# Performance work log

Measured on AMD Instinct MI355X. Metric: run time of the kernel, lower is better.

## Reference

```python
import jax, jax.numpy as jnp
import numpy as np

C = 128; PE = 8; WALK = 20; NODE_F = 28; EDGE_F = 4
L = 4; H = 4; DH = C // H; B = 64; NPG = 512; N = B * NPG; E = 262144
BN_EPS = 1e-5


def _bn(x, g, b):
    # BatchNorm1d, training-mode statistics (biased var), over the node axis
    m = x.mean(0)
    v = x.var(0)
    return (x - m) * jax.lax.rsqrt(v + BN_EPS) * g + b


def _forward(pe, node_emb, pe_lin_w, pe_lin_b, pe_norm_g, pe_norm_b, edge_emb,
             gine_w1, gine_b1, gine_w2, gine_b2,
             attn_wqkv, attn_bqkv, attn_wo, attn_bo,
             norm1_g, norm1_b, norm2_g, norm2_b, norm3_g, norm3_b,
             ffn_w1, ffn_b1, ffn_w2, ffn_b2,
             mlp_w1, mlp_b1, mlp_w2, mlp_b2, mlp_w3, mlp_b3,
             x, edge_index, edge_attr, batch):
    pe_n = _bn(pe, pe_norm_g, pe_norm_b)
    h = jnp.concatenate([node_emb[x[:, 0]], pe_n @ pe_lin_w + pe_lin_b], axis=1)  # [N, C]
    ea = edge_emb[edge_attr]  # [E, C]
    src, dst = edge_index[0], edge_index[1]
    scale = 1.0 / jnp.sqrt(jnp.asarray(DH, h.dtype))
    for l in range(L):
        # --- GINEConv: nn((1+eps)*x + sum_{j->i} relu(x_j + e_ji)), eps=0 ---
        msg = jax.nn.relu(h[src] + ea)                      # [E, C] gather
        agg = jax.ops.segment_sum(msg, dst, num_segments=N) # [N, C] scatter-add
        z = agg + h
        local = jax.nn.relu(z @ gine_w1[l] + gine_b1[l]) @ gine_w2[l] + gine_b2[l]
        h_loc = _bn(local + h, norm1_g[l], norm1_b[l])
        # --- global multihead attention on dense batch [B, NPG, C] (equal-size graphs) ---
        xd = h.reshape(B, NPG, C)
        qkv = xd @ attn_wqkv[l] + attn_bqkv[l]              # [B, NPG, 3C]
        q, k, v = jnp.split(qkv, 3, axis=-1)
        q = q.reshape(B, NPG, H, DH)
        k = k.reshape(B, NPG, H, DH)
        v = v.reshape(B, NPG, H, DH)
        att = jax.nn.softmax(jnp.einsum('bqhd,bkhd->bhqk', q, k) * scale, axis=-1)
        o = jnp.einsum('bhqk,bkhd->bqhd', att, v).reshape(B, NPG, C) @ attn_wo[l] + attn_bo[l]
        h_att = _bn(o.reshape(N, C) + h, norm2_g[l], norm2_b[l])
        # --- combine + FFN (GPSConv) ---
        out = h_loc + h_att
        ffn = jax.nn.relu(out @ ffn_w1[l] + ffn_b1[l]) @ ffn_w2[l] + ffn_b2[l]
        h = _bn(out + ffn, norm3_g[l], norm3_b[l])
    g = jax.ops.segment_sum(h, batch, num_segments=B)       # global_add_pool -> [B, C]
    y = jax.nn.relu(g @ mlp_w1 + mlp_b1)
    y = jax.nn.relu(y @ mlp_w2 + mlp_b2)
    return y @ mlp_w3 + mlp_b3                              # [B, 1]


def setup_inputs() -> dict:
    key = jax.random.key(0)
    ks = iter(jax.random.split(key, 48))
    def w(shape, s=0.05):
        return jax.random.normal(next(ks), shape, jnp.float32) * s
    inp = {}
    inp['x'] = jax.random.randint(next(ks), (N, 1), 0, NODE_F)
    inp['pe'] = jax.random.normal(next(ks), (N, WALK), jnp.float32)
    inp['edge_index'] = jax.random.randint(next(ks), (2, E), 0, N)
    inp['edge_attr'] = jax.random.randint(next(ks), (E,), 0, EDGE_F)
    inp['batch'] = jnp.arange(N, dtype=jnp.int32) // NPG
    inp['node_emb'] = w((NODE_F, C - PE), 1.0)
    inp['pe_lin_w'] = w((WALK, PE))
    inp['pe_lin_b'] = jnp.zeros((PE,), jnp.float32)
    inp['pe_norm_g'] = jnp.ones((WALK,), jnp.float32)
    inp['pe_norm_b'] = jnp.zeros((WALK,), jnp.float32)
    inp['edge_emb'] = w((EDGE_F, C), 1.0)
    inp['gine_w1'] = w((L, C, C))
    inp['gine_b1'] = jnp.zeros((L, C), jnp.float32)
    inp['gine_w2'] = w((L, C, C))
    inp['gine_b2'] = jnp.zeros((L, C), jnp.float32)
    inp['attn_wqkv'] = w((L, C, 3 * C))
    inp['attn_bqkv'] = jnp.zeros((L, 3 * C), jnp.float32)
    inp['attn_wo'] = w((L, C, C))
    inp['attn_bo'] = jnp.zeros((L, C), jnp.float32)
    for nm in ('norm1', 'norm2', 'norm3'):
        inp[nm + '_g'] = jnp.ones((L, C), jnp.float32)
        inp[nm + '_b'] = jnp.zeros((L, C), jnp.float32)
    inp['ffn_w1'] = w((L, C, 2 * C))
    inp['ffn_b1'] = jnp.zeros((L, 2 * C), jnp.float32)
    inp['ffn_w2'] = w((L, 2 * C, C))
    inp['ffn_b2'] = jnp.zeros((L, C), jnp.float32)
    inp['mlp_w1'] = w((C, C // 2))
    inp['mlp_b1'] = jnp.zeros((C // 2,), jnp.float32)
    inp['mlp_w2'] = w((C // 2, C // 4))
    inp['mlp_b2'] = jnp.zeros((C // 4,), jnp.float32)
    inp['mlp_w3'] = w((C // 4, 1))
    inp['mlp_b3'] = jnp.zeros((1,), jnp.float32)
    return inp


def reference(x, pe, edge_index, edge_attr, batch,
              node_emb, pe_lin_w, pe_lin_b, pe_norm_g, pe_norm_b, edge_emb,
              gine_w1, gine_b1, gine_w2, gine_b2,
              attn_wqkv, attn_bqkv, attn_wo, attn_bo,
              norm1_g, norm1_b, norm2_g, norm2_b, norm3_g, norm3_b,
              ffn_w1, ffn_b1, ffn_w2, ffn_b2,
              mlp_w1, mlp_b1, mlp_w2, mlp_b2, mlp_w3, mlp_b3):
    return _forward(pe, node_emb, pe_lin_w, pe_lin_b, pe_norm_g, pe_norm_b, edge_emb,
                    gine_w1, gine_b1, gine_w2, gine_b2,
                    attn_wqkv, attn_bqkv, attn_wo, attn_bo,
                    norm1_g, norm1_b, norm2_g, norm2_b, norm3_g, norm3_b,
                    ffn_w1, ffn_b1, ffn_w2, ffn_b2,
                    mlp_w1, mlp_b1, mlp_w2, mlp_b2, mlp_w3, mlp_b3,
                    x, edge_index, edge_attr, batch)
```

## Files before the change

kernel.cpp:

```cpp
#include <hip/hip_runtime.h>
#include <math.h>
#include <cstddef>

#define N_NODES 32768
#define C_DIM   128
#define E_EDGES 262144
#define B_GR    64
#define NPG     512
#define WALK_D  20
#define L_LAYERS 4

static constexpr int NF = N_NODES * C_DIM;

typedef __attribute__((ext_vector_type(8))) short bf16x8;
typedef __attribute__((ext_vector_type(4))) float f32x4;
typedef __attribute__((ext_vector_type(4))) short short4v;

__device__ inline unsigned short f2bf(float f)
{
    union { float f; unsigned u; } v; v.f = f;
    unsigned r = v.u + 0x7fff + ((v.u >> 16) & 1);
    return (unsigned short)(r >> 16);
}
__device__ inline float bf2f_lo(unsigned u) { return __uint_as_float(u << 16); }
__device__ inline float bf2f_hi(unsigned u) { return __uint_as_float(u & 0xffff0000u); }
__device__ inline unsigned cvt_pk_bf16(float lo, float hi)
{
    unsigned r;
    asm("v_cvt_pk_bf16_f32 %0, %1, %2" : "=v"(r) : "v"(lo), "v"(hi));
    return r;
}

__global__ __launch_bounds__(256) void pe_stats_k(const float* __restrict__ pe, float* __restrict__ acc)
{
    int gt = blockIdx.x * 256 + threadIdx.x;
    float s[WALK_D], q[WALK_D];
    #pragma unroll
    for (int c = 0; c < WALK_D; ++c) { s[c] = 0.f; q[c] = 0.f; }
    for (int r = 0; r < 4; ++r) {
        const float* row = &pe[(size_t)(gt + r * 8192) * WALK_D];
        float v[20];
        #pragma unroll
        for (int j = 0; j < 5; ++j) *(float4*)&v[j * 4] = *(const float4*)(row + j * 4);
        #pragma unroll
        for (int c = 0; c < WALK_D; ++c) { s[c] += v[c]; q[c] += v[c] * v[c]; }
    }
    #pragma unroll
    for (int c = 0; c < WALK_D; ++c) {
        float ss = s[c], qq = q[c];
        #pragma unroll
        for (int m = 1; m < 64; m <<= 1) { ss += __shfl_xor(ss, m); qq += __shfl_xor(qq, m); }
        if ((threadIdx.x & 63) == 0) { atomicAdd(&acc[c], ss); atomicAdd(&acc[32 + c], qq); }
    }
}

__global__ __launch_bounds__(256) void h0_k(const int* __restrict__ x, const float* __restrict__ pe,
    const float* __restrict__ node_emb, const float* __restrict__ plw, const float* __restrict__ plb,
    const float* __restrict__ peacc, const float* __restrict__ pe_g, const float* __restrict__ pe_b,
    float* __restrict__ h, unsigned short* __restrict__ h16)
{
    __shared__ float spe[64];
    int tid = threadIdx.x;
    if (tid < WALK_D) {
        float mean = peacc[tid] * (1.f / N_NODES);
        float var  = peacc[32 + tid] * (1.f / N_NODES) - mean * mean;
        float sc   = pe_g[tid] * rsqrtf(var + 1e-5f);
        spe[tid] = sc;
        spe[32 + tid] = pe_b[tid] - mean * sc;
    }
    __syncthreads();
    int i = blockIdx.x * 2 + (tid >> 7);
    int c = tid & 127;
    float v;
    if (c < 120) {
        v = node_emb[x[i] * 120 + c];
    } else {
        int pc = c - 120;
        v = plb[pc];
        #pragma unroll
        for (int k = 0; k < WALK_D; ++k) {
            float pn = pe[i * WALK_D + k] * spe[k] + spe[32 + k];
            v = fmaf(pn, plw[k * 8 + pc], v);
        }
    }
    h[i * C_DIM + c] = v;
    h16[i * C_DIM + c] = f2bf(v);
}

__global__ __launch_bounds__(256) void hist_k(const int* __restrict__ dst, int* __restrict__ cnt)
{
    int e = blockIdx.x * 256 + threadIdx.x;
    atomicAdd(&cnt[dst[e]], 1);
}

__global__ __launch_bounds__(256) void bsum_k(const int* __restrict__ cnt, int* __restrict__ bsum)
{
    __shared__ int ws[4];
    int b = blockIdx.x, t = threadIdx.x;
    int v = cnt[b * 256 + t];
    #pragma unroll
    for (int m = 1; m < 64; m <<= 1) v += __shfl_xor(v, m);
    if ((t & 63) == 0) ws[t >> 6] = v;
    __syncthreads();
    if (t == 0) bsum[b] = ws[0] + ws[1] + ws[2] + ws[3];
}

__global__ __launch_bounds__(128) void bscan_k(const int* __restrict__ bsum, int* __restrict__ bpre)
{
    __shared__ int s[128];
    int t = threadIdx.x;
    int v = bsum[t];
    s[t] = v;
    __syncthreads();
    for (int off = 1; off < 128; off <<= 1) {
        int u = (t >= off) ? s[t - off] : 0;
        __syncthreads();
        s[t] += u;
        __syncthreads();
    }
    bpre[t] = s[t] - v;
}

__global__ __launch_bounds__(256) void indptr_k(const int* __restrict__ cnt, const int* __restrict__ bpre,
                                                int* __restrict__ indptr)
{
    __shared__ int s[256];
    int b = blockIdx.x, t = threadIdx.x;
    int v = cnt[b * 256 + t];
    s[t] = v;
    __syncthreads();
    for (int off = 1; off < 256; off <<= 1) {
        int u = (t >= off) ? s[t - off] : 0;
        __syncthreads();
        s[t] += u;
        __syncthreads();
    }
    indptr[b * 256 + t] = bpre[b] + s[t] - v;
    if (b == 127 && t == 255) indptr[N_NODES] = E_EDGES;
}

__global__ __launch_bounds__(256) void scatter_k(const int* __restrict__ dst, const int* __restrict__ src,
                                                 const int* __restrict__ attr, const int* __restrict__ indptr,
                                                 int* __restrict__ cur, int* __restrict__ esa)
{
    int e = blockIdx.x * 256 + threadIdx.x;
    int d = dst[e];
    int pos = atomicAdd(&cur[d], 1);
    esa[indptr[d] + pos] = src[e] | (attr[e] << 16);
}

__global__ __launch_bounds__(256) void gine_gather_k(const unsigned short* __restrict__ h16,
    const int* __restrict__ esa, const int* __restrict__ indptr,
    const float* __restrict__ edge_emb, unsigned short* __restrict__ z16)
{
    __shared__ float ee[4 * C_DIM];
    int tid = threadIdx.x;
    ee[tid] = edge_emb[tid];
    ee[tid + 256] = edge_emb[tid + 256];
    __syncthreads();
    int i = blockIdx.x * 4 + (tid >> 6);
    int c = (tid & 63) * 2;
    int p0 = indptr[i], p1 = indptr[i + 1];
    float s0 = 0.f, s1 = 0.f;
    int p = p0;
    for (; p + 4 <= p1; p += 4) {
        int sa0 = esa[p], sa1 = esa[p + 1], sa2 = esa[p + 2], sa3 = esa[p + 3];
        unsigned u0 = *(const unsigned*)&h16[(size_t)(sa0 & 0xffff) * C_DIM + c];
        unsigned u1 = *(const unsigned*)&h16[(size_t)(sa1 & 0xffff) * C_DIM + c];
        unsigned u2 = *(const unsigned*)&h16[(size_t)(sa2 & 0xffff) * C_DIM + c];
        unsigned u3 = *(const unsigned*)&h16[(size_t)(sa3 & 0xffff) * C_DIM + c];
        float2 e0 = *(const float2*)&ee[(sa0 >> 16) * C_DIM + c];
        float2 e1 = *(const float2*)&ee[(sa1 >> 16) * C_DIM + c];
        float2 e2 = *(const float2*)&ee[(sa2 >> 16) * C_DIM + c];
        float2 e3 = *(const float2*)&ee[(sa3 >> 16) * C_DIM + c];
        s0 += fmaxf(bf2f_lo(u0) + e0.x, 0.f); s1 += fmaxf(bf2f_hi(u0) + e0.y, 0.f);
        s0 += fmaxf(bf2f_lo(u1) + e1.x, 0.f); s1 += fmaxf(bf2f_hi(u1) + e1.y, 0.f);
        s0 += fmaxf(bf2f_lo(u2) + e2.x, 0.f); s1 += fmaxf(bf2f_hi(u2) + e2.y, 0.f);
        s0 += fmaxf(bf2f_lo(u3) + e3.x, 0.f); s1 += fmaxf(bf2f_hi(u3) + e3.y, 0.f);
    }
    for (; p < p1; ++p) {
        int sa = esa[p];
        unsigned u = *(const unsigned*)&h16[(size_t)(sa & 0xffff) * C_DIM + c];
        float2 ev = *(const float2*)&ee[(sa >> 16) * C_DIM + c];
        s0 += fmaxf(bf2f_lo(u) + ev.x, 0.f);
        s1 += fmaxf(bf2f_hi(u) + ev.y, 0.f);
    }
    unsigned us = *(const unsigned*)&h16[(size_t)i * C_DIM + c];
    s0 += bf2f_lo(us);
    s1 += bf2f_hi(us);
    *(unsigned*)&z16[(size_t)i * C_DIM + c] = cvt_pk_bf16(s0, s1);
}

__global__ __launch_bounds__(256) void wt_prep_k(
    const float* __restrict__ gw1, const float* __restrict__ gw2,
    const float* __restrict__ wqkv, const float* __restrict__ wo,
    const float* __restrict__ fw1, const float* __restrict__ fw2,
    short* __restrict__ out)
{
    __shared__ float ts[32][36];
    int b = blockIdx.x;
    int l = b / 160, t = b % 160;
    const float* src; int K, N; size_t obase; int tile;
    if (t < 16)       { src = gw1  + (size_t)l * 16384; K = 128; N = 128; obase = (size_t)l * 163840 + 0;      tile = t; }
    else if (t < 32)  { src = gw2  + (size_t)l * 16384; K = 128; N = 128; obase = (size_t)l * 163840 + 16384;  tile = t - 16; }
    else if (t < 80)  { src = wqkv + (size_t)l * 49152; K = 128; N = 384; obase = (size_t)l * 163840 + 32768;  tile = t - 32; }
    else if (t < 96)  { src = wo   + (size_t)l * 16384; K = 128; N = 128; obase = (size_t)l * 163840 + 81920;  tile = t - 80; }
    else if (t < 128) { src = fw1  + (size_t)l * 32768; K = 128; N = 256; obase = (size_t)l * 163840 + 98304;  tile = t - 96; }
    else              { src = fw2  + (size_t)l * 32768; K = 256; N = 128; obase = (size_t)l * 163840 + 131072; tile = t - 128; }
    int ntN = N / 32;
    int tk = tile / ntN, tn = tile % ntN;
    int tid = threadIdx.x;
    int r = tid >> 3, c4 = (tid & 7) * 4;
    *(float4*)&ts[r][c4] = *(const float4*)&src[(size_t)(tk * 32 + r) * N + tn * 32 + c4];
    __syncthreads();
    int n = tid >> 3, k4 = (tid & 7) * 4;
    short4v pk;
    #pragma unroll
    for (int i2 = 0; i2 < 4; ++i2) pk[i2] = (short)f2bf(ts[k4 + i2][n]);
    *(short4v*)&out[obase + (size_t)(tn * 32 + n) * K + tk * 32 + k4] = pk;
}

template<int KD, int NC, int AMODE, int RESMODE, bool RELU, bool STATS, bool OUTBF, bool ABF, bool VOUT>
__global__ __launch_bounds__(256) void mgemm_k(
    const void* __restrict__ Av, const float* __restrict__ A2,
    const float* __restrict__ affA1, const float* __restrict__ affA2,
    const unsigned short* __restrict__ Bt, const float* __restrict__ bias,
    const float* __restrict__ R1, const float* __restrict__ R2,
    const float* __restrict__ affR1, const float* __restrict__ affR2,
    void* __restrict__ Cout, float* __restrict__ stats,
    unsigned short* __restrict__ vtg)
{
    __shared__ short As[16384];
    __shared__ short Bs[8192];
    const int tid = threadIdx.x;
    const int w = tid >> 6;
    const int lane = tid & 63;
    const int lr = lane & 15, lg = lane >> 4;
    const int row0 = blockIdx.y * 128;
    const int col0 = blockIdx.x * 128;

    const f32x4 zero = {0.f, 0.f, 0.f, 0.f};
    f32x4 acc[2][8];
    #pragma unroll
    for (int i = 0; i < 2; ++i)
        #pragma unroll
        for (int cf = 0; cf < 8; ++cf) acc[i][cf] = zero;

    for (int kt = 0; kt < KD / 128; ++kt) {
        if (kt > 0) __syncthreads();
        #pragma unroll
        for (int it = 0; it < 8; ++it) {
            int gid = it * 256 + tid;
            int row = gid >> 4, g = gid & 15;
            bf16x8 pk;
            if (ABF) {
                pk = *(const bf16x8*)&((const unsigned short*)Av)[(size_t)(row0 + row) * KD + kt * 128 + g * 8];
            } else {
                const float* Af = (const float*)Av;
                const float* ap = &Af[(size_t)(row0 + row) * KD + kt * 128 + g * 8];
                float v[8];
                *(float4*)&v[0] = *(const float4*)ap;
                *(float4*)&v[4] = *(const float4*)(ap + 4);
                if (AMODE == 1) {
                    const float* ap2 = &A2[(size_t)(row0 + row) * KD + kt * 128 + g * 8];
                    float u[8];
                    *(float4*)&u[0] = *(const float4*)ap2;
                    *(float4*)&u[4] = *(const float4*)(ap2 + 4);
                    #pragma unroll
                    for (int j = 0; j < 8; ++j) {
                        int ck = g * 8 + j;
                        v[j] = v[j] * affA1[ck] + affA1[128 + ck] + u[j] * affA2[ck] + affA2[128 + ck];
                    }
                }
                #pragma unroll
                for (int j = 0; j < 8; ++j) pk[j] = (short)f2bf(v[j]);
            }
            *(bf16x8*)&As[(row * 16 + (g ^ (row & 7))) * 8] = pk;
        }
        #pragma unroll
        for (int h = 0; h < 2; ++h) {
            if (h > 0) __syncthreads();
            #pragma unroll
            for (int it = 0; it < 4; ++it) {
                int gid = it * 256 + tid;
                int row = gid >> 4, g = gid & 15;
                bf16x8 bv = *(const bf16x8*)&Bt[(size_t)(col0 + h * 64 + row) * KD + kt * 128 + g * 8];
                *(bf16x8*)&Bs[(row * 16 + (g ^ (row & 7))) * 8] = bv;
            }
            __syncthreads();
            #pragma unroll
            for (int ks = 0; ks < 4; ++ks) {
                bf16x8 af[2], bfr[4];
                #pragma unroll
                for (int i = 0; i < 2; ++i) {
                    int row = w * 32 + i * 16 + lr;
                    int g = ks * 4 + lg;
                    af[i] = *(const bf16x8*)&As[(row * 16 + (g ^ (row & 7))) * 8];
                }
                #pragma unroll
                for (int cfl = 0; cfl < 4; ++cfl) {
                    int lc = cfl * 16 + lr;
                    int g = ks * 4 + lg;
                    bfr[cfl] = *(const bf16x8*)&Bs[(lc * 16 + (g ^ (lc & 7))) * 8];
                }
                #pragma unroll
                for (int i = 0; i < 2; ++i)
                    #pragma unroll
                    for (int cfl = 0; cfl < 4; ++cfl)
                        acc[i][h * 4 + cfl] = __builtin_amdgcn_mfma_f32_16x16x32_bf16(af[i], bfr[cfl], acc[i][h * 4 + cfl], 0, 0, 0);
            }
        }
    }

    float* cs = (float*)As;
    float* cq = cs + 128;
    if (STATS) {
        __syncthreads();
        if (tid < 128) { cs[tid] = 0.f; cq[tid] = 0.f; }
        __syncthreads();
    }
    float bs_v[8];
    #pragma unroll
    for (int cf = 0; cf < 8; ++cf) bs_v[cf] = bias[col0 + cf * 16 + lr];
    float rs1[8], ro1[8], rs2[8], ro2[8];
    if (RESMODE == 2) {
        #pragma unroll
        for (int cf = 0; cf < 8; ++cf) {
            int c = cf * 16 + lr;
            rs1[cf] = affR1[c]; ro1[cf] = affR1[128 + c];
            rs2[cf] = affR2[c]; ro2[cf] = affR2[128 + c];
        }
    }
    float colS[8], colQ[8];
    #pragma unroll
    for (int cf = 0; cf < 8; ++cf) { colS[cf] = 0.f; colQ[cf] = 0.f; }
    const bool vblk = VOUT && (col0 == 256);
    #pragma unroll
    for (int i = 0; i < 2; ++i) {
        #pragma unroll
        for (int r = 0; r < 4; ++r) {
            size_t grow = row0 + w * 32 + i * 16 + lg * 4 + r;
            #pragma unroll
            for (int cf = 0; cf < 8; ++cf) {
                int c = col0 + cf * 16 + lr;
                float val = acc[i][cf][r] + bs_v[cf];
                if (RESMODE == 1) val += R1[grow * NC + c];
                if (RESMODE == 2) {
                    val += R1[grow * 128 + c] * rs1[cf] + ro1[cf]
                         + R2[grow * 128 + c] * rs2[cf] + ro2[cf];
                }
                if (RELU) val = fmaxf(val, 0.f);
                if (VOUT && vblk) {
                    int g2 = (int)(grow >> 9);
                    int key = (int)(grow & 511);
                    int kc = key >> 6, kg = (key >> 3) & 7, j = key & 7;
                    int cd = c - 256;
                    int hd2 = cd >> 5, dd = cd & 31;
                    vtg[((size_t)(g2 * 4 + hd2) * 8 + kc) * 2048 + dd * 64 + ((kg ^ (dd & 7)) << 3) + j] = f2bf(val);
                } else if (OUTBF) {
                    ((unsigned short*)Cout)[grow * NC + c] = f2bf(val);
                } else {
                    ((float*)Cout)[grow * NC + c] = val;
                }
                if (STATS) { colS[cf] += val; colQ[cf] += val * val; }
            }
        }
    }
    if (STATS) {
        #pragma unroll
        for (int cf = 0; cf < 8; ++cf) {
            float s = colS[cf], q = colQ[cf];
            s += __shfl_xor(s, 16); s += __shfl_xor(s, 32);
            q += __shfl_xor(q, 16); q += __shfl_xor(q, 32);
            if (lg == 0) { atomicAdd(&cs[cf * 16 + lr], s); atomicAdd(&cq[cf * 16 + lr], q); }
        }
        __syncthreads();
        if (tid < 128) {
            atomicAdd(&stats[tid], cs[tid]);
            atomicAdd(&stats[128 + tid], cq[tid]);
        }
    }
}

__global__ __launch_bounds__(512) void gine_mlp_k(
    const unsigned short* __restrict__ z16,
    const unsigned short* __restrict__ W1t, const float* __restrict__ b1,
    const unsigned short* __restrict__ W2t, const float* __restrict__ b2,
    const float* __restrict__ Hres,
    float* __restrict__ T1out, float* __restrict__ stats)
{
    __shared__ short As[16384];
    __shared__ short Bs[16384];
    const int tid = threadIdx.x;
    const int w = tid >> 6;
    const int lane = tid & 63;
    const int lr = lane & 15, lg = lane >> 4;
    const int row0 = blockIdx.x * 128;
    const f32x4 zero = {0.f, 0.f, 0.f, 0.f};
    const int arow = w * 16 + lr;

    #pragma unroll
    for (int it = 0; it < 4; ++it) {
        int gid = it * 512 + tid;
        int row = gid >> 4, g = gid & 15;
        bf16x8 av = *(const bf16x8*)&z16[(size_t)(row0 + row) * 128 + g * 8];
        *(bf16x8*)&As[(row * 16 + (g ^ (row & 7))) * 8] = av;
        bf16x8 bv = *(const bf16x8*)&W1t[(size_t)row * 128 + g * 8];
        *(bf16x8*)&Bs[(row * 16 + (g ^ (row & 7))) * 8] = bv;
    }
    __syncthreads();

    f32x4 acc[8];
    #pragma unroll
    for (int cf = 0; cf < 8; ++cf) acc[cf] = zero;
    #pragma unroll
    for (int ks = 0; ks < 4; ++ks) {
        int g = ks * 4 + lg;
        bf16x8 af = *(const bf16x8*)&As[(arow * 16 + (g ^ (arow & 7))) * 8];
        #pragma unroll
        for (int cf = 0; cf < 8; ++cf) {
            int c = cf * 16 + lr;
            bf16x8 bfr = *(const bf16x8*)&Bs[(c * 16 + (g ^ (c & 7))) * 8];
            acc[cf] = __builtin_amdgcn_mfma_f32_16x16x32_bf16(af, bfr, acc[cf], 0, 0, 0);
        }
    }
    __syncthreads();

    {
        float bias1[8];
        #pragma unroll
        for (int cf = 0; cf < 8; ++cf) bias1[cf] = b1[cf * 16 + lr];
        #pragma unroll
        for (int r = 0; r < 4; ++r) {
            int row = w * 16 + lg * 4 + r;
            #pragma unroll
            for (int cf = 0; cf < 8; ++cf) {
                int col = cf * 16 + lr;
                float val = fmaxf(acc[cf][r] + bias1[cf], 0.f);
                As[(row * 16 + ((col >> 3) ^ (row & 7))) * 8 + (col & 7)] = (short)f2bf(val);
            }
        }
    }
    #pragma unroll
    for (int it = 0; it < 4; ++it) {
        int gid = it * 512 + tid;
        int row = gid >> 4, g = gid & 15;
        bf16x8 bv = *(const bf16x8*)&W2t[(size_t)row * 128 + g * 8];
        *(bf16x8*)&Bs[(row * 16 + (g ^ (row & 7))) * 8] = bv;
    }
    __syncthreads();

    #pragma unroll
    for (int cf = 0; cf < 8; ++cf) acc[cf] = zero;
    #pragma unroll
    for (int ks = 0; ks < 4; ++ks) {
        int g = ks * 4 + lg;
        bf16x8 af = *(const bf16x8*)&As[(arow * 16 + (g ^ (arow & 7))) * 8];
        #pragma unroll
        for (int cf = 0; cf < 8; ++cf) {
            int c = cf * 16 + lr;
            bf16x8 bfr = *(const bf16x8*)&Bs[(c * 16 + (g ^ (c & 7))) * 8];
            acc[cf] = __builtin_amdgcn_mfma_f32_16x16x32_bf16(af, bfr, acc[cf], 0, 0, 0);
        }
    }

    float* cs = (float*)As;
    float* cq = cs + 128;
    __syncthreads();
    if (tid < 128) { cs[tid] = 0.f; cq[tid] = 0.f; }
    __syncthreads();
    float bs_v[8];
    #pragma unroll
    for (int cf = 0; cf < 8; ++cf) bs_v[cf] = b2[cf * 16 + lr];
    float colS[8], colQ[8];
    #pragma unroll
    for (int cf = 0; cf < 8; ++cf) { colS[cf] = 0.f; colQ[cf] = 0.f; }
    #pragma unroll
    for (int r = 0; r < 4; ++r) {
        size_t grow = row0 + w * 16 + lg * 4 + r;
        #pragma unroll
        for (int cf = 0; cf < 8; ++cf) {
            int c = cf * 16 + lr;
            float val = acc[cf][r] + bs_v[cf] + Hres[grow * 128 + c];
            T1out[grow * 128 + c] = val;
            colS[cf] += val; colQ[cf] += val * val;
        }
    }
    #pragma unroll
    for (int cf = 0; cf < 8; ++cf) {
        float s = colS[cf], q = colQ[cf];
        s += __shfl_xor(s, 16); s += __shfl_xor(s, 32);
        q += __shfl_xor(q, 16); q += __shfl_xor(q, 32);
        if (lg == 0) { atomicAdd(&cs[cf * 16 + lr], s); atomicAdd(&cq[cf * 16 + lr], q); }
    }
    __syncthreads();
    if (tid < 128) {
        atomicAdd(&stats[tid], cs[tid]);
        atomicAdd(&stats[128 + tid], cq[tid]);
    }
}

__global__ __launch_bounds__(256) void ffn_mlp_k(
    const float* __restrict__ T1, const float* __restrict__ T2,
    const float* __restrict__ a1, const float* __restrict__ g1v, const float* __restrict__ b1v,
    const float* __restrict__ a2, const float* __restrict__ g2v, const float* __restrict__ b2v,
    const unsigned short* __restrict__ W1t, const float* __restrict__ fb1,
    const unsigned short* __restrict__ W2t, const float* __restrict__ fb2,
    float* __restrict__ T1out, float* __restrict__ stats)
{
    __shared__ short As[8192];
    __shared__ short Bs[16384];
    __shared__ short Ys[8192];
    __shared__ float sf1l[256], sf2l[256];
    const int tid = threadIdx.x;
    const int w = tid >> 6;
    const int lane = tid & 63;
    const int lr = lane & 15, lg = lane >> 4;
    const int row0 = blockIdx.x * 64;
    const f32x4 zero = {0.f, 0.f, 0.f, 0.f};

    if (tid < 128) {
        float mean = a1[tid] * (1.f / N_NODES);
        float var  = a1[128 + tid] * (1.f / N_NODES) - mean * mean;
        float sc   = g1v[tid] * rsqrtf(var + 1e-5f);
        sf1l[tid] = sc; sf1l[128 + tid] = b1v[tid] - mean * sc;
        mean = a2[tid] * (1.f / N_NODES);
        var  = a2[128 + tid] * (1.f / N_NODES) - mean * mean;
        sc   = g2v[tid] * rsqrtf(var + 1e-5f);
        sf2l[tid] = sc; sf2l[128 + tid] = b2v[tid] - mean * sc;
    }
    __syncthreads();

    #pragma unroll
    for (int it = 0; it < 4; ++it) {
        int gid = it * 256 + tid;
        int row = gid >> 4, g = gid & 15;
        const float* ap = &T1[(size_t)(row0 + row) * 128 + g * 8];
        const float* ap2 = &T2[(size_t)(row0 + row) * 128 + g * 8];
        float v[8], u[8];
        *(float4*)&v[0] = *(const float4*)ap;
        *(float4*)&v[4] = *(const float4*)(ap + 4);
        *(float4*)&u[0] = *(const float4*)ap2;
        *(float4*)&u[4] = *(const float4*)(ap2 + 4);
        unsigned pw[4];
        #pragma unroll
        for (int j2 = 0; j2 < 4; ++j2) {
            int ck0 = g * 8 + j2 * 2, ck1 = ck0 + 1;
            float x0 = v[j2 * 2]     * sf1l[ck0] + sf1l[128 + ck0] + u[j2 * 2]     * sf2l[ck0] + sf2l[128 + ck0];
            float x1 = v[j2 * 2 + 1] * sf1l[ck1] + sf1l[128 + ck1] + u[j2 * 2 + 1] * sf2l[ck1] + sf2l[128 + ck1];
            pw[j2] = cvt_pk_bf16(x0, x1);
        }
        *(uint4*)&As[(row * 16 + (g ^ (row & 7))) * 8] = *(uint4*)pw;
    }

    f32x4 acc2[8];
    #pragma unroll
    for (int cf = 0; cf < 8; ++cf) acc2[cf] = zero;

    const int arow = w * 16 + lr;
    for (int h = 0; h < 2; ++h) {
        if (h > 0) __syncthreads();
        #pragma unroll
        for (int it = 0; it < 8; ++it) {
            int gid = it * 256 + tid;
            int row = gid >> 4, g = gid & 15;
            bf16x8 bv = *(const bf16x8*)&W1t[(size_t)(h * 128 + row) * 128 + g * 8];
            *(bf16x8*)&Bs[(row * 16 + (g ^ (row & 7))) * 8] = bv;
        }
        __syncthreads();
        f32x4 accY[8];
        #pragma unroll
        for (int cf = 0; cf < 8; ++cf) accY[cf] = zero;
        #pragma unroll
        for (int ks = 0; ks < 4; ++ks) {
            int g = ks * 4 + lg;
            bf16x8 af = *(const bf16x8*)&As[(arow * 16 + (g ^ (arow & 7))) * 8];
            #pragma unroll
            for (int cf = 0; cf < 8; ++cf) {
                int c = cf * 16 + lr;
                bf16x8 bfr = *(const bf16x8*)&Bs[(c * 16 + (g ^ (c & 7))) * 8];
                accY[cf] = __builtin_amdgcn_mfma_f32_16x16x32_bf16(af, bfr, accY[cf], 0, 0, 0);
            }
        }
        __syncthreads();
        #pragma unroll
        for (int r = 0; r < 4; ++r) {
            int row = w * 16 + lg * 4 + r;
            #pragma unroll
            for (int cf = 0; cf < 8; ++cf) {
                int col = cf * 16 + lr;
                float val = fmaxf(accY[cf][r] + fb1[h * 128 + col], 0.f);
                Ys[(row * 16 + ((col >> 3) ^ (row & 7))) * 8 + (col & 7)] = (short)f2bf(val);
            }
        }
        #pragma unroll
        for (int it = 0; it < 8; ++it) {
            int gid = it * 256 + tid;
            int row = gid >> 4, g = gid & 15;
            bf16x8 bv = *(const bf16x8*)&W2t[(size_t)row * 256 + h * 128 + g * 8];
            *(bf16x8*)&Bs[(row * 16 + (g ^ (row & 7))) * 8] = bv;
        }
        __syncthreads();
        #pragma unroll
        for (int ks = 0; ks < 4; ++ks) {
            int g = ks * 4 + lg;
            bf16x8 af = *(const bf16x8*)&Ys[(arow * 16 + (g ^ (arow & 7))) * 8];
            #pragma unroll
            for (int cf = 0; cf < 8; ++cf) {
                int c = cf * 16 + lr;
                bf16x8 bfr = *(const bf16x8*)&Bs[(c * 16 + (g ^ (c & 7))) * 8];
                acc2[cf] = __builtin_amdgcn_mfma_f32_16x16x32_bf16(af, bfr, acc2[cf], 0, 0, 0);
            }
        }
    }

    float* cs = (float*)As;
    float* cq = cs + 128;
    __syncthreads();
    if (tid < 128) { cs[tid] = 0.f; cq[tid] = 0.f; }
    __syncthreads();
    float bs_v[8], rs1[8], ro1[8], rs2[8], ro2[8];
    #pragma unroll
    for (int cf = 0; cf < 8; ++cf) {
        int c = cf * 16 + lr;
        bs_v[cf] = fb2[c];
        rs1[cf] = sf1l[c]; ro1[cf] = sf1l[128 + c];
        rs2[cf] = sf2l[c]; ro2[cf] = sf2l[128 + c];
    }
    float colS[8], colQ[8];
    #pragma unroll
    for (int cf = 0; cf < 8; ++cf) { colS[cf] = 0.f; colQ[cf] = 0.f; }
    #pragma unroll
    for (int r = 0; r < 4; ++r) {
        size_t grow = row0 + w * 16 + lg * 4 + r;
        #pragma unroll
        for (int cf = 0; cf < 8; ++cf) {
            int c = cf * 16 + lr;
            float val = acc2[cf][r] + bs_v[cf]
                      + T1[grow * 128 + c] * rs1[cf] + ro1[cf]
                      + T2[grow * 128 + c] * rs2[cf] + ro2[cf];
            T1out[grow * 128 + c] = val;
            colS[cf] += val; colQ[cf] += val * val;
        }
    }
    #pragma unroll
    for (int cf = 0; cf < 8; ++cf) {
        float s = colS[cf], q = colQ[cf];
        s += __shfl_xor(s, 16); s += __shfl_xor(s, 32);
        q += __shfl_xor(q, 16); q += __shfl_xor(q, 32);
        if (lg == 0) { atomicAdd(&cs[cf * 16 + lr], s); atomicAdd(&cq[cf * 16 + lr], q); }
    }
    __syncthreads();
    if (tid < 128) {
        atomicAdd(&stats[tid], cs[tid]);
        atomicAdd(&stats[128 + tid], cq[tid]);
    }
}

__global__ __launch_bounds__(256) void attn_mfma_k(const unsigned short* __restrict__ qkvb,
                                                   const unsigned short* __restrict__ vtg,
                                                   unsigned short* __restrict__ ao16)
{
    __shared__ short Qs[2048];
    __shared__ short Ks[2][2048];
    __shared__ short Vs[2][2048];
    __shared__ short Ps[4][1024];
    const int tid = threadIdx.x;
    const int w = tid >> 6, lane = tid & 63;
    const int lr = lane & 15, lg = lane >> 4;
    const int q0 = blockIdx.x * 64;
    const int hd = blockIdx.y;
    const int base = blockIdx.z * NPG;
    const float SCL = 0.17677669529663687f * 1.44269504089f;
    const f32x4 zero = {0.f, 0.f, 0.f, 0.f};
    const unsigned short* vbase = vtg + (size_t)(blockIdx.z * 4 + hd) * 16384;

    {
        int row = tid >> 2, g = tid & 3;
        bf16x8 qv = *(const bf16x8*)&qkvb[(size_t)(base + q0 + row) * 384 + hd * 32 + g * 8];
        *(bf16x8*)&Qs[(row * 4 + (g ^ ((row >> 1) & 3))) * 8] = qv;
        bf16x8 kv = *(const bf16x8*)&qkvb[(size_t)(base + row) * 384 + 128 + hd * 32 + g * 8];
        *(bf16x8*)&Ks[0][(row * 4 + (g ^ ((row >> 1) & 3))) * 8] = kv;
        bf16x8 vv = *(const bf16x8*)&vbase[tid * 8];
        *(bf16x8*)&Vs[0][tid * 8] = vv;
    }
    __syncthreads();
    const int qrow = w * 16 + lr;
    const bf16x8 bq = *(const bf16x8*)&Qs[(qrow * 4 + (lg ^ ((qrow >> 1) & 3))) * 8];
    float m = -1e30f, lsum = 0.f;
    f32x4 o[2];
    o[0] = zero; o[1] = zero;

    for (int kc = 0; kc < 8; ++kc) {
        int buf = kc & 1;
        bf16x8 knx, vnx;
        if (kc < 7) {
            int row = tid >> 2, g = tid & 3;
            knx = *(const bf16x8*)&qkvb[(size_t)(base + (kc + 1) * 64 + row) * 384 + 128 + hd * 32 + g * 8];
            vnx = *(const bf16x8*)&vbase[(size_t)(kc + 1) * 2048 + tid * 8];
        }
        bf16x8 ka[4], va[2][2];
        #pragma unroll
        for (int kf = 0; kf < 4; ++kf) {
            int kr = kf * 16 + lr;
            ka[kf] = *(const bf16x8*)&Ks[buf][(kr * 4 + (lg ^ ((kr >> 1) & 3))) * 8];
        }
        #pragma unroll
        for (int ks = 0; ks < 2; ++ks)
            #pragma unroll
            for (int df = 0; df < 2; ++df) {
                int d = df * 16 + lr;
                int kg = ks * 4 + lg;
                va[ks][df] = *(const bf16x8*)&Vs[buf][(d * 8 + (kg ^ (d & 7))) * 8];
            }
        f32x4 s[4];
        #pragma unroll
        for (int kf = 0; kf < 4; ++kf)
            s[kf] = __builtin_amdgcn_mfma_f32_16x16x32_bf16(ka[kf], bq, zero, 0, 0, 0);
        float v[16];
        #pragma unroll
        for (int kf = 0; kf < 4; ++kf)
            #pragma unroll
            for (int r = 0; r < 4; ++r) v[kf * 4 + r] = s[kf][r] * SCL;
        float rm = fmaxf(fmaxf(fmaxf(fmaxf(v[0], v[1]), fmaxf(v[2], v[3])),
                               fmaxf(fmaxf(v[4], v[5]), fmaxf(v[6], v[7]))),
                         fmaxf(fmaxf(fmaxf(v[8], v[9]), fmaxf(v[10], v[11])),
                               fmaxf(fmaxf(v[12], v[13]), fmaxf(v[14], v[15]))));
        rm = fmaxf(rm, __shfl_xor(rm, 16));
        rm = fmaxf(rm, __shfl_xor(rm, 32));
        float mn = fmaxf(m, rm);
        float alpha = exp2f(m - mn);
        float p[16];
        #pragma unroll
        for (int i = 0; i < 16; ++i) p[i] = exp2f(v[i] - mn);
        float S0 = ((p[0] + p[4]) + p[8]) + p[12];
        float S1 = ((p[1] + p[5]) + p[9]) + p[13];
        float S2 = ((p[2] + p[6]) + p[10]) + p[14];
        float S3 = ((p[3] + p[7]) + p[11]) + p[15];
        float ps = (S0 + S1) + (S2 + S3);
        ps += __shfl_xor(ps, 16);
        ps += __shfl_xor(ps, 32);
        lsum = lsum * alpha + ps;
        m = mn;
        o[0] *= alpha;
        o[1] *= alpha;
        #pragma unroll
        for (int kf = 0; kf < 4; ++kf) {
            uint2 pk;
            pk.x = cvt_pk_bf16(p[kf * 4 + 0], p[kf * 4 + 1]);
            pk.y = cvt_pk_bf16(p[kf * 4 + 2], p[kf * 4 + 3]);
            int gr = (kf * 2 + (lg >> 1)) ^ (lr & 7);
            *(uint2*)&Ps[w][lr * 64 + gr * 8 + (lg & 1) * 4] = pk;
        }
        #pragma unroll
        for (int ks = 0; ks < 2; ++ks) {
            bf16x8 pa = *(const bf16x8*)&Ps[w][lr * 64 + (((ks * 4 + lg) ^ (lr & 7))) * 8];
            #pragma unroll
            for (int df = 0; df < 2; ++df)
                o[df] = __builtin_amdgcn_mfma_f32_16x16x32_bf16(va[ks][df], pa, o[df], 0, 0, 0);
        }
        if (kc < 7) {
            int row = tid >> 2, g = tid & 3;
            *(bf16x8*)&Ks[buf ^ 1][(row * 4 + (g ^ ((row >> 1) & 3))) * 8] = knx;
            *(bf16x8*)&Vs[buf ^ 1][tid * 8] = vnx;
        }
        __syncthreads();
    }
    {
        float inv = 1.f / lsum;
        size_t nrow = (size_t)base + q0 + w * 16 + lr;
        #pragma unroll
        for (int df = 0; df < 2; ++df) {
            uint2 ov;
            ov.x = cvt_pk_bf16(o[df][0] * inv, o[df][1] * inv);
            ov.y = cvt_pk_bf16(o[df][2] * inv, o[df][3] * inv);
            *(uint2*)&ao16[nrow * 128 + hd * 32 + df * 16 + lg * 4] = ov;
        }
    }
}

__global__ __launch_bounds__(256) void bn_apply_k(const float* __restrict__ t,
    const float* __restrict__ a3, const float* __restrict__ g3, const float* __restrict__ b3,
    float* __restrict__ h, unsigned short* __restrict__ h16)
{
    __shared__ float sfl[256];
    int tid = threadIdx.x;
    if (tid < 128) {
        float mean = a3[tid] * (1.f / N_NODES);
        float var  = a3[128 + tid] * (1.f / N_NODES) - mean * mean;
        float sc   = g3[tid] * rsqrtf(var + 1e-5f);
        sfl[tid] = sc;
        sfl[128 + tid] = b3[tid] - mean * sc;
    }
    __syncthreads();
    int idx = blockIdx.x * 256 + tid;
    int cg = (idx & 31) * 4;
    float4 v  = *(const float4*)&t[idx * 4];
    float4 sc = *(const float4*)&sfl[cg];
    float4 sh = *(const float4*)&sfl[128 + cg];
    float4 o;
    o.x = v.x * sc.x + sh.x;
    o.y = v.y * sc.y + sh.y;
    o.z = v.z * sc.z + sh.z;
    o.w = v.w * sc.w + sh.w;
    *(float4*)&h[idx * 4] = o;
    uint2 p;
    p.x = cvt_pk_bf16(o.x, o.y);
    p.y = cvt_pk_bf16(o.z, o.w);
    *(uint2*)&h16[idx * 4] = p;
}

__global__ __launch_bounds__(128) void pool_k(const float* __restrict__ h, float* __restrict__ g)
{
    int b = blockIdx.x, c = threadIdx.x;
    float s = 0.f;
    for (int i = 0; i < NPG; ++i) s += h[(size_t)((b << 9) + i) * C_DIM + c];
    g[b * C_DIM + c] = s;
}

__global__ __launch_bounds__(256) void head_mlp_k(const float* __restrict__ g,
    const float* __restrict__ w1, const float* __restrict__ b1,
    const float* __restrict__ w2, const float* __restrict__ b2,
    const float* __restrict__ w3, const float* __restrict__ b3,
    float* __restrict__ out)
{
    __shared__ float gs[64 * 128];
    __shared__ float y1[64 * 64];
    __shared__ float y2[64 * 32];
    int tid = threadIdx.x;
    for (int r = 0; r < 32; ++r) gs[r * 256 + tid] = g[r * 256 + tid];
    __syncthreads();
    for (int t = 0; t < 16; ++t) {
        int idx = t * 256 + tid;
        int gi = idx >> 6, c = idx & 63;
        float s = b1[c];
        for (int k = 0; k < 128; ++k) s = fmaf(gs[gi * 128 + k], w1[k * 64 + c], s);
        y1[gi * 64 + c] = fmaxf(s, 0.f);
    }
    __syncthreads();
    for (int t = 0; t < 8; ++t) {
        int idx = t * 256 + tid;
        int gi = idx >> 5, c = idx & 31;
        float s = b2[c];
        for (int k = 0; k < 64; ++k) s = fmaf(y1[gi * 64 + k], w2[k * 32 + c], s);
        y2[gi * 32 + c] = fmaxf(s, 0.f);
    }
    __syncthreads();
    if (tid < 64) {
        float s = b3[0];
        for (int k = 0; k < 32; ++k) s = fmaf(y2[tid * 32 + k], w3[k], s);
        out[tid] = s;
    }
}

extern "C" void kernel_launch(void* const* d_in, const int* in_sizes, int n_in,
                              void* d_out, int out_size, void* d_ws, size_t ws_size,
                              hipStream_t stream)
{
    const int*   x        = (const int*)  d_in[0];
    const float* pe       = (const float*)d_in[1];
    const int*   ei       = (const int*)  d_in[2];
    const int*   eattr    = (const int*)  d_in[3];
    const float* node_emb = (const float*)d_in[5];
    const float* plw      = (const float*)d_in[6];
    const float* plb      = (const float*)d_in[7];
    const float* pe_g     = (const float*)d_in[8];
    const float* pe_b     = (const float*)d_in[9];
    const float* edge_emb = (const float*)d_in[10];
    const float* gw1      = (const float*)d_in[11];
    const float* gb1      = (const float*)d_in[12];
    const float* gw2      = (const float*)d_in[13];
    const float* gb2      = (const float*)d_in[14];
    const float* wqkv     = (const float*)d_in[15];
    const float* bqkv     = (const float*)d_in[16];
    const float* wo       = (const float*)d_in[17];
    const float* bo       = (const float*)d_in[18];
    const float* n1g      = (const float*)d_in[19];
    const float* n1b      = (const float*)d_in[20];
    const float* n2g      = (const float*)d_in[21];
    const float* n2b      = (const float*)d_in[22];
    const float* n3g      = (const float*)d_in[23];
    const float* n3b      = (const float*)d_in[24];
    const float* fw1      = (const float*)d_in[25];
    const float* fb1      = (const float*)d_in[26];
    const float* fw2      = (const float*)d_in[27];
    const float* fb2      = (const float*)d_in[28];
    const float* mw1      = (const float*)d_in[29];
    const float* mb1      = (const float*)d_in[30];
    const float* mw2      = (const float*)d_in[31];
    const float* mb2      = (const float*)d_in[32];
    const float* mw3      = (const float*)d_in[33];
    const float* mb3      = (const float*)d_in[34];

    float* wf  = (float*)d_ws;
    float* Hb  = wf;
    unsigned short* Zb16 = (unsigned short*)(wf + (size_t)NF);
    float* T1  = wf + 2 * (size_t)NF;
    unsigned short* QKVb = (unsigned short*)(wf + 3 * (size_t)NF);
    float* T2  = wf + 3 * (size_t)NF;
    unsigned short* vtg = (unsigned short*)(wf + 4 * (size_t)NF + (size_t)NF / 2);
    unsigned short* Hb16 = (unsigned short*)(wf + 5 * (size_t)NF);
    int* wi     = (int*)(wf + 6 * (size_t)NF);
    int* indptr = wi;
    int* cnt    = wi + 32800;
    int* cnt2   = cnt + N_NODES;
    int* bsum   = cnt2 + N_NODES;
    int* bpre   = bsum + 128;
    int* esa    = bpre + 128;
    float* st    = (float*)(esa + E_EDGES);
    float* peacc = st;
    float* bnacc = st + 64;
    float* gpool = bnacc + 12 * 256;
    short* wT    = (short*)(gpool + 64 * 128);

    const int* srcA = ei;
    const int* dstA = ei + E_EDGES;
    const int LSTR = 163840;

    hipMemsetAsync(peacc, 0, (64 + 12 * 256) * sizeof(float), stream);
    hipMemsetAsync(cnt, 0, 2 * N_NODES * sizeof(int), stream);

    wt_prep_k<<<640, 256, 0, stream>>>(gw1, gw2, wqkv, wo, fw1, fw2, wT);
    pe_stats_k<<<32, 256, 0, stream>>>(pe, peacc);
    h0_k<<<N_NODES / 2, 256, 0, stream>>>(x, pe, node_emb, plw, plb, peacc, pe_g, pe_b, Hb, Hb16);
    hist_k<<<E_EDGES / 256, 256, 0, stream>>>(dstA, cnt);
    bsum_k<<<128, 256, 0, stream>>>(cnt, bsum);
    bscan_k<<<1, 128, 0, stream>>>(bsum, bpre);
    indptr_k<<<128, 256, 0, stream>>>(cnt, bpre, indptr);
    scatter_k<<<E_EDGES / 256, 256, 0, stream>>>(dstA, srcA, eattr, indptr, cnt2, esa);

    for (int l = 0; l < L_LAYERS; ++l) {
        const short* gw1t  = wT + (size_t)l * LSTR;
        const short* gw2t  = wT + (size_t)l * LSTR + 16384;
        const short* wqkvt = wT + (size_t)l * LSTR + 32768;
        const short* wot   = wT + (size_t)l * LSTR + 81920;
        const short* fw1t  = wT + (size_t)l * LSTR + 98304;
        const short* fw2t  = wT + (size_t)l * LSTR + 131072;
        const float* lgb1  = gb1 + (size_t)l * 128;
        const float* lgb2  = gb2 + (size_t)l * 128;
        const float* lbqkv = bqkv + (size_t)l * 384;
        const float* lbo   = bo + (size_t)l * 128;
        const float* lfb1  = fb1 + (size_t)l * 256;
        const float* lfb2  = fb2 + (size_t)l * 128;
        float* acc1 = bnacc + (l * 3 + 0) * 256;
        float* acc2 = bnacc + (l * 3 + 1) * 256;
        float* acc3 = bnacc + (l * 3 + 2) * 256;

        gine_gather_k<<<N_NODES / 4, 256, 0, stream>>>(Hb16, esa, indptr, edge_emb, Zb16);
        gine_mlp_k<<<256, 512, 0, stream>>>(
            Zb16, (const unsigned short*)gw1t, lgb1, (const unsigned short*)gw2t, lgb2,
            Hb, T1, acc1);
        mgemm_k<128, 384, 0, 0, false, false, true,  true, true ><<<dim3(3, 256), 256, 0, stream>>>(
            Hb16, nullptr, nullptr, nullptr, (const unsigned short*)wqkvt, lbqkv,
            nullptr, nullptr, nullptr, nullptr, QKVb, nullptr, vtg);
        attn_mfma_k<<<dim3(8, 4, 64), 256, 0, stream>>>(QKVb, vtg, Zb16);
        mgemm_k<128, 128, 0, 1, false, true,  false, true, false><<<dim3(1, 256), 256, 0, stream>>>(
            Zb16, nullptr, nullptr, nullptr, (const unsigned short*)wot, lbo,
            Hb, nullptr, nullptr, nullptr, T2, acc2, nullptr);
        ffn_mlp_k<<<512, 256, 0, stream>>>(
            T1, T2,
            acc1, n1g + l * 128, n1b + l * 128,
            acc2, n2g + l * 128, n2b + l * 128,
            (const unsigned short*)fw1t, lfb1, (const unsigned short*)fw2t, lfb2,
            T1, acc3);
        bn_apply_k<<<NF / 1024, 256, 0, stream>>>(T1, acc3, n3g + l * 128, n3b + l * 128, Hb, Hb16);
    }
    pool_k<<<B_GR, 128, 0, stream>>>(Hb, gpool);
    head_mlp_k<<<1, 256, 0, stream>>>(gpool, mw1, mb1, mw2, mb2, mw3, mb3, (float*)d_out);
}
```

Baseline: 700.4 us.

## Merge GINE edge gather and QKV projection GEMM into one heterogeneous kernel

Replaces the separate gather launch and QKV GEMM launch with a single kernel whose first 768 blocks run the QKV MFMA GEMM and whose remaining 8192 blocks run the neighbor gather. Both read only the bf16 node features, so they can run concurrently and the compute-bound GEMM overlaps the latency-bound gather. This also removes one launch per layer. The cost is 48KB of shared memory for every block, including gather blocks that need only 2KB, which may lower occupancy for the gather part.

New measurement: 766.2 us. +9.4%, slower.

```diff
diff --git a/kernel.cpp b/kernel.cpp
--- a/kernel.cpp
+++ b/kernel.cpp
@@ -147,48 +147,6 @@
     int d = dst[e];
     int pos = atomicAdd(&cur[d], 1);
     esa[indptr[d] + pos] = src[e] | (attr[e] << 16);
-}
-
-__global__ __launch_bounds__(256) void gine_gather_k(const unsigned short* __restrict__ h16,
-    const int* __restrict__ esa, const int* __restrict__ indptr,
-    const float* __restrict__ edge_emb, unsigned short* __restrict__ z16)
-{
-    __shared__ float ee[4 * C_DIM];
-    int tid = threadIdx.x;
-    ee[tid] = edge_emb[tid];
-    ee[tid + 256] = edge_emb[tid + 256];
-    __syncthreads();
-    int i = blockIdx.x * 4 + (tid >> 6);
-    int c = (tid & 63) * 2;
-    int p0 = indptr[i], p1 = indptr[i + 1];
-    float s0 = 0.f, s1 = 0.f;
-    int p = p0;
-    for (; p + 4 <= p1; p += 4) {
-        int sa0 = esa[p], sa1 = esa[p + 1], sa2 = esa[p + 2], sa3 = esa[p + 3];
-        unsigned u0 = *(const unsigned*)&h16[(size_t)(sa0 & 0xffff) * C_DIM + c];
-        unsigned u1 = *(const unsigned*)&h16[(size_t)(sa1 & 0xffff) * C_DIM + c];
-        unsigned u2 = *(const unsigned*)&h16[(size_t)(sa2 & 0xffff) * C_DIM + c];
-        unsigned u3 = *(const unsigned*)&h16[(size_t)(sa3 & 0xffff) * C_DIM + c];
-        float2 e0 = *(const float2*)&ee[(sa0 >> 16) * C_DIM + c];
-        float2 e1 = *(const float2*)&ee[(sa1 >> 16) * C_DIM + c];
-        float2 e2 = *(const float2*)&ee[(sa2 >> 16) * C_DIM + c];
-        float2 e3 = *(const float2*)&ee[(sa3 >> 16) * C_DIM + c];
-        s0 += fmaxf(bf2f_lo(u0) + e0.x, 0.f); s1 += fmaxf(bf2f_hi(u0) + e0.y, 0.f);
-        s0 += fmaxf(bf2f_lo(u1) + e1.x, 0.f); s1 += fmaxf(bf2f_hi(u1) + e1.y, 0.f);
-        s0 += fmaxf(bf2f_lo(u2) + e2.x, 0.f); s1 += fmaxf(bf2f_hi(u2) + e2.y, 0.f);
-        s0 += fmaxf(bf2f_lo(u3) + e3.x, 0.f); s1 += fmaxf(bf2f_hi(u3) + e3.y, 0.f);
-    }
-    for (; p < p1; ++p) {
-        int sa = esa[p];
-        unsigned u = *(const unsigned*)&h16[(size_t)(sa & 0xffff) * C_DIM + c];
-        float2 ev = *(const float2*)&ee[(sa >> 16) * C_DIM + c];
-        s0 += fmaxf(bf2f_lo(u) + ev.x, 0.f);
-        s1 += fmaxf(bf2f_hi(u) + ev.y, 0.f);
-    }
-    unsigned us = *(const unsigned*)&h16[(size_t)i * C_DIM + c];
-    s0 += bf2f_lo(us);
-    s1 += bf2f_hi(us);
-    *(unsigned*)&z16[(size_t)i * C_DIM + c] = cvt_pk_bf16(s0, s1);
 }
 
 __global__ __launch_bounds__(256) void wt_prep_k(
@@ -218,6 +176,135 @@
     #pragma unroll
     for (int i2 = 0; i2 < 4; ++i2) pk[i2] = (short)f2bf(ts[k4 + i2][n]);
     *(short4v*)&out[obase + (size_t)(tn * 32 + n) * K + tk * 32 + k4] = pk;
+}
+
+__global__ __launch_bounds__(256) void gq_k(
+    const unsigned short* __restrict__ h16,
+    const int* __restrict__ esa, const int* __restrict__ indptr,
+    const float* __restrict__ edge_emb, unsigned short* __restrict__ z16,
+    const unsigned short* __restrict__ Bt, const float* __restrict__ bias,
+    unsigned short* __restrict__ qkvb, unsigned short* __restrict__ vtg)
+{
+    __shared__ char smem[49152];
+    const int tid = threadIdx.x;
+    if (blockIdx.x < 768) {
+        short* As = (short*)smem;
+        short* Bs = (short*)(smem + 32768);
+        const int w = tid >> 6;
+        const int lane = tid & 63;
+        const int lr = lane & 15, lg = lane >> 4;
+        const int col0 = (blockIdx.x % 3) * 128;
+        const int row0 = (blockIdx.x / 3) * 128;
+        const f32x4 zero = {0.f, 0.f, 0.f, 0.f};
+        f32x4 acc[2][8];
+        #pragma unroll
+        for (int i = 0; i < 2; ++i)
+            #pragma unroll
+            for (int cf = 0; cf < 8; ++cf) acc[i][cf] = zero;
+
+        #pragma unroll
+        for (int it = 0; it < 8; ++it) {
+            int gid = it * 256 + tid;
+            int row = gid >> 4, g = gid & 15;
+            bf16x8 pk = *(const bf16x8*)&h16[(size_t)(row0 + row) * 128 + g * 8];
+            *(bf16x8*)&As[(row * 16 + (g ^ (row & 7))) * 8] = pk;
+        }
+        #pragma unroll
+        for (int h = 0; h < 2; ++h) {
+            if (h > 0) __syncthreads();
+            #pragma unroll
+            for (int it = 0; it < 4; ++it) {
+                int gid = it * 256 + tid;
+                int row = gid >> 4, g = gid & 15;
+                bf16x8 bv = *(const bf16x8*)&Bt[(size_t)(col0 + h * 64 + row) * 128 + g * 8];
+                *(bf16x8*)&Bs[(row * 16 + (g ^ (row & 7))) * 8] = bv;
+            }
+            __syncthreads();
+            #pragma unroll
+            for (int ks = 0; ks < 4; ++ks) {
+                bf16x8 af[2], bfr[4];
+                #pragma unroll
+                for (int i = 0; i < 2; ++i) {
+                    int row = w * 32 + i * 16 + lr;
+                    int g = ks * 4 + lg;
+                    af[i] = *(const bf16x8*)&As[(row * 16 + (g ^ (row & 7))) * 8];
+                }
+                #pragma unroll
+                for (int cfl = 0; cfl < 4; ++cfl) {
+                    int lc = cfl * 16 + lr;
+                    int g = ks * 4 + lg;
+                    bfr[cfl] = *(const bf16x8*)&Bs[(lc * 16 + (g ^ (lc & 7))) * 8];
+                }
+                #pragma unroll
+                for (int i = 0; i < 2; ++i)
+                    #pragma unroll
+                    for (int cfl = 0; cfl < 4; ++cfl)
+                        acc[i][h * 4 + cfl] = __builtin_amdgcn_mfma_f32_16x16x32_bf16(af[i], bfr[cfl], acc[i][h * 4 + cfl], 0, 0, 0);
+            }
+        }
+        float bs_v[8];
+        #pragma unroll
+        for (int cf = 0; cf < 8; ++cf) bs_v[cf] = bias[col0 + cf * 16 + lr];
+        const bool vblk = (col0 == 256);
+        #pragma unroll
+        for (int i = 0; i < 2; ++i) {
+            #pragma unroll
+            for (int r = 0; r < 4; ++r) {
+                size_t grow = row0 + w * 32 + i * 16 + lg * 4 + r;
+                #pragma unroll
+                for (int cf = 0; cf < 8; ++cf) {
+                    int c = col0 + cf * 16 + lr;
+                    float val = acc[i][cf][r] + bs_v[cf];
+                    if (vblk) {
+                        int g2 = (int)(grow >> 9);
+                        int key = (int)(grow & 511);
+                        int kc = key >> 6, kg = (key >> 3) & 7, j = key & 7;
+                        int cd = c - 256;
+                        int hd2 = cd >> 5, dd = cd & 31;
+                        vtg[((size_t)(g2 * 4 + hd2) * 8 + kc) * 2048 + dd * 64 + ((kg ^ (dd & 7)) << 3) + j] = f2bf(val);
+                    } else {
+                        qkvb[grow * 384 + c] = f2bf(val);
+                    }
+                }
+            }
+        }
+    } else {
+        float* ee = (float*)smem;
+        ee[tid] = edge_emb[tid];
+        ee[tid + 256] = edge_emb[tid + 256];
+        __syncthreads();
+        int i = (blockIdx.x - 768) * 4 + (tid >> 6);
+        int c = (tid & 63) * 2;
+        int p0 = indptr[i], p1 = indptr[i + 1];
+        float s0 = 0.f, s1 = 0.f;
+        int p = p0;
+        for (; p + 4 <= p1; p += 4) {
+            int sa0 = esa[p], sa1 = esa[p + 1], sa2 = esa[p + 2], sa3 = esa[p + 3];
+            unsigned u0 = *(const unsigned*)&h16[(size_t)(sa0 & 0xffff) * C_DIM + c];
+            unsigned u1 = *(const unsigned*)&h16[(size_t)(sa1 & 0xffff) * C_DIM + c];
+            unsigned u2 = *(const unsigned*)&h16[(size_t)(sa2 & 0xffff) * C_DIM + c];
+            unsigned u3 = *(const unsigned*)&h16[(size_t)(sa3 & 0xffff) * C_DIM + c];
+            float2 e0 = *(const float2*)&ee[(sa0 >> 16) * C_DIM + c];
+            float2 e1 = *(const float2*)&ee[(sa1 >> 16) * C_DIM + c];
+            float2 e2 = *(const float2*)&ee[(sa2 >> 16) * C_DIM + c];
+            float2 e3 = *(const float2*)&ee[(sa3 >> 16) * C_DIM + c];
+            s0 += fmaxf(bf2f_lo(u0) + e0.x, 0.f); s1 += fmaxf(bf2f_hi(u0) + e0.y, 0.f);
+            s0 += fmaxf(bf2f_lo(u1) + e1.x, 0.f); s1 += fmaxf(bf2f_hi(u1) + e1.y, 0.f);
+            s0 += fmaxf(bf2f_lo(u2) + e2.x, 0.f); s1 += fmaxf(bf2f_hi(u2) + e2.y, 0.f);
+            s0 += fmaxf(bf2f_lo(u3) + e3.x, 0.f); s1 += fmaxf(bf2f_hi(u3) + e3.y, 0.f);
+        }
+        for (; p < p1; ++p) {
+            int sa = esa[p];
+            unsigned u = *(const unsigned*)&h16[(size_t)(sa & 0xffff) * C_DIM + c];
+            float2 ev = *(const float2*)&ee[(sa >> 16) * C_DIM + c];
+            s0 += fmaxf(bf2f_lo(u) + ev.x, 0.f);
+            s1 += fmaxf(bf2f_hi(u) + ev.y, 0.f);
+        }
+        unsigned us = *(const unsigned*)&h16[(size_t)i * C_DIM + c];
+        s0 += bf2f_lo(us);
+        s1 += bf2f_hi(us);
+        *(unsigned*)&z16[(size_t)i * C_DIM + c] = cvt_pk_bf16(s0, s1);
+    }
 }
 
 template<int KD, int NC, int AMODE, int RESMODE, bool RELU, bool STATS, bool OUTBF, bool ABF, bool VOUT>
@@ -946,13 +1033,12 @@
         float* acc2 = bnacc + (l * 3 + 1) * 256;
         float* acc3 = bnacc + (l * 3 + 2) * 256;
 
-        gine_gather_k<<<N_NODES / 4, 256, 0, stream>>>(Hb16, esa, indptr, edge_emb, Zb16);
+        gq_k<<<8960, 256, 0, stream>>>(
+            Hb16, esa, indptr, edge_emb, Zb16,
+            (const unsigned short*)wqkvt, lbqkv, QKVb, vtg);
         gine_mlp_k<<<256, 512, 0, stream>>>(
             Zb16, (const unsigned short*)gw1t, lgb1, (const unsigned short*)gw2t, lgb2,
             Hb, T1, acc1);
-        mgemm_k<128, 384, 0, 0, false, false, true,  true, true ><<<dim3(3, 256), 256, 0, stream>>>(
-            Hb16, nullptr, nullptr, nullptr, (const unsigned short*)wqkvt, lbqkv,
-            nullptr, nullptr, nullptr, nullptr, QKVb, nullptr, vtg);
         attn_mfma_k<<<dim3(8, 4, 64), 256, 0, stream>>>(QKVb, vtg, Zb16);
         mgemm_k<128, 128, 0, 1, false, true,  false, true, false><<<dim3(1, 256), 256, 0, stream>>>(
             Zb16, nullptr, nullptr, nullptr, (const unsigned short*)wot, lbo,
```
